# Optimization experiments

Measured on AMD Instinct MI355X. Metric: run time of the kernel, lower is better.

## Reference

```python
import jax, jax.numpy as jnp
import numpy as np

HEADS = 16
SEGS = 8


def _rotate_half(x):
    x1, x2 = jnp.split(x, 2, axis=-1)
    return jnp.concatenate([-x2, x1], axis=-1)


def _split_heads(t, h):
    b, n, dim = t.shape
    d = dim // h
    return t.reshape(b, n, h, d).transpose(0, 2, 1, 3).reshape(b * h, n, d)


def _merge_heads(t, b, h):
    c, n, d = t.shape
    return t.reshape(b, h, n, d).transpose(0, 2, 1, 3).reshape(b, n, h * d)


def setup_inputs() -> dict:
    key = jax.random.key(0)
    ks = jax.random.split(key, 5)
    b, n, dim = 2, 4096, 1024
    x = jax.random.normal(ks[0], (b, n, dim), dtype=jnp.float32)
    w = lambda k: jax.random.normal(k, (dim, dim), dtype=jnp.float32) * 0.02
    return {
        'x': x,
        'Wq': w(ks[1]),
        'Wkv': w(ks[2]),
        'Wo': w(ks[3]),
        'bo': jnp.zeros((dim,), jnp.float32),
        'Wo0': w(ks[4]),
        'bo0': jnp.zeros((dim,), jnp.float32),
    }


def reference(x, Wq, Wkv, Wo, bo, Wo0, bo0):
    b, n, dim = x.shape
    h = HEADS
    d = dim // h
    s = SEGS
    m = n // s  # segment_len
    mask_value = -jnp.finfo(x.dtype).max

    q = _split_heads(x @ Wq, h)    # (b*h, n, d)
    kv = _split_heads(x @ Wkv, h)  # (b*h, n, d)  (serves as both keys and values)

    # rotary embedding (layer_num == 0 branch)
    inv_freq = 1.0 / (10000.0 ** (jnp.arange(0, d, 2, dtype=jnp.float32) / d))
    freqs = jnp.arange(n, dtype=jnp.float32)[:, None] * inv_freq[None, :]  # (n, d/2)
    rot = jnp.concatenate([freqs, freqs], axis=-1)[None]  # (1, n, d)
    cos, sin = jnp.cos(rot), jnp.sin(rot)
    q = q * cos + _rotate_half(q) * sin
    kv = kv * cos + _rotate_half(kv) * sin

    q = q * (d ** -0.5)

    qs = q.reshape(-1, s, m, d)   # (c, s, m, d)
    kvs = kv.reshape(-1, s, m, d)

    # overlapping windows: segment t paired with segment t+1 as kv context
    kvs_ccs = jnp.concatenate([kvs[:, :-1], kvs[:, 1:]], axis=2)  # (c, s-1, 2m, d)
    qs_ccs = qs[:, 1:]                                            # (c, s-1, m, d)

    # NOTE: original computes lkv = LayerNorm(kvs_ccs) but never uses it (dead code) -> omitted.

    lsim = jnp.einsum('csmd,csnd->csmn', qs_ccs, kvs_ccs)  # (c, s-1, m, 2m)
    causal = jnp.triu(jnp.ones((m, m), dtype=bool), 1)
    # causal mask only applied to second half of keys (the own segment t+1)
    lsim = jnp.concatenate(
        [lsim[..., :m], jnp.where(causal, mask_value, lsim[..., m:])], axis=-1)

    attn0 = jnp.einsum('csmd,csnd->csmn', qs[:, :1], kvs[:, :1])  # (c, 1, m, m)
    attn0 = jnp.where(causal, mask_value, attn0)

    attn0 = jax.nn.softmax(attn0, axis=-1)
    attn1 = jax.nn.softmax(lsim, axis=-1)

    out0 = jnp.einsum('csij,csjd->csid', attn0, kvs[:, :1]).reshape(-1, m, d)
    out1 = jnp.einsum('csij,csjd->csid', attn1, kvs_ccs).reshape(-1, (s - 1) * m, d)

    out0 = _merge_heads(out0, b, h) @ Wo0 + bo0  # (b, m, dim)
    out1 = _merge_heads(out1, b, h) @ Wo + bo    # (b, (s-1)*m, dim)
    return jnp.concatenate([out0, out1], axis=1)  # (b, n, dim)
```

## Files before the change

### kernel.cpp

```cpp
#include <hip/hip_runtime.h>
#include <hip/hip_bf16.h>
#include <float.h>

using bf16 = __hip_bfloat16;
typedef __attribute__((ext_vector_type(8))) short bf16x8;
typedef __attribute__((ext_vector_type(4))) float f32x4;
typedef __attribute__((ext_vector_type(16))) float f32x16;

#define DIM   1024
#define NSEQ  4096
#define BATCH 2
#define NH    16
#define HD    64
#define NSEG  8
#define MSEG  512
#define ROWS  (BATCH*NSEQ)
#define NC    (BATCH*NH)
#define QSCALE (0.125f * 1.44269504f)

__device__ __forceinline__ float fast_exp2(float x) {
    float r;
    asm volatile("v_exp_f32 %0, %1" : "=v"(r) : "v"(x));
    return r;
}

__device__ __forceinline__ void gload16(const bf16* g, bf16* l) {
    __builtin_amdgcn_global_load_lds((const __attribute__((address_space(1))) unsigned int*)g,
                                     (__attribute__((address_space(3))) unsigned int*)l, 16, 0, 0);
}

__global__ void k_prep(const float* __restrict__ x, bf16* __restrict__ Xb,
                       const float* __restrict__ Wq, const float* __restrict__ Wkv,
                       const float* __restrict__ Wo, const float* __restrict__ Wo0,
                       bf16* __restrict__ WqT, bf16* __restrict__ WkvT,
                       bf16* __restrict__ WoT, bf16* __restrict__ Wo0T,
                       float* __restrict__ cosT, float* __restrict__ sinT) {
    __shared__ float tile[32][33];
    int b = blockIdx.x, tid = threadIdx.x;
    if (b < 8192) {
        int i = (b * 256 + tid) * 4;
        float4 v = *(const float4*)&x[i];
        union { bf16 h[4]; uint2 u; } p;
        p.h[0] = __float2bfloat16(v.x);
        p.h[1] = __float2bfloat16(v.y);
        p.h[2] = __float2bfloat16(v.z);
        p.h[3] = __float2bfloat16(v.w);
        *(uint2*)&Xb[i] = p.u;
    } else if (b < 12288) {
        int zz = (b - 8192) >> 10;
        int bb = (b - 8192) & 1023;
        int bxt = (bb & 31) * 32, byt = (bb >> 5) * 32;
        const float* W = (zz == 0) ? Wq : (zz == 1) ? Wkv : (zz == 2) ? Wo : Wo0;
        bf16* Wt = (zz == 0) ? WqT : (zz == 1) ? WkvT : (zz == 2) ? WoT : Wo0T;
        int tx = tid & 31, ty = tid >> 5;
        for (int ii = ty; ii < 32; ii += 8)
            tile[ii][tx] = W[(size_t)(byt + ii) * DIM + bxt + tx];
        __syncthreads();
        for (int ii = ty; ii < 32; ii += 8)
            Wt[(size_t)(bxt + ii) * DIM + byt + tx] = __float2bfloat16(tile[tx][ii]);
    } else {
        int idx = (b - 12288) * 256 + tid;
        int t = idx >> 5, ii = idx & 31;
        float freq = 1.0f / powf(10000.0f, (float)(2 * ii) * (1.0f / 64.0f));
        float a = (float)t * freq;
        cosT[idx] = cosf(a);
        sinT[idx] = sinf(a);
    }
}

__launch_bounds__(256, 3)
__global__ void k_gemm_qkv(const bf16* __restrict__ A, const bf16* __restrict__ Bq,
                           const bf16* __restrict__ Bkv, const float* __restrict__ cosT,
                           const float* __restrict__ sinT, bf16* __restrict__ Qb,
                           bf16* __restrict__ KVf) {
    __shared__ alignas(16) bf16 SH[24576];
    bf16* AsB = SH;
    bf16* BsB = SH + 12288;
    const int K = DIM;
    int tid = threadIdx.x;
    int lane = tid & 63, wave = tid >> 6;
    int hi = lane >> 5, lq = lane & 31;
    int wr = (wave >> 1) * 64, wc = (wave & 1) * 64;
    int id = blockIdx.x;
    int xcd = id & 7, rank = id >> 3;
    int by = xcd * 8 + (rank >> 4);
    int bxx = rank & 15;
    int m0 = by * 128;
    bool isQ = (bxx < 8);
    const bf16* Bt = isQ ? Bq : Bkv;
    int n0 = (bxx & 7) * 128;
    int row = lane & 15, kk = (lane >> 4) * 8;
    int kkA = kk ^ (((lane >> 1) & 3) << 3);
    int ch0 = wave * 128 + lane, ch1 = ch0 + 64;
    int r0 = ch0 >> 2, c0e = (ch0 & 3) * 8;
    int r1 = ch1 >> 2, c1e = (ch1 & 3) * 8;
    int c0s = c0e ^ (((r0 >> 1) & 3) << 3);
    int c1s = c1e ^ (((r1 >> 1) & 3) << 3);
    f32x4 acc[4][4] = {};

    auto stage = [&](int k0, int b) {
        gload16(&A[(size_t)(m0 + r0) * K + k0 + c0s], &AsB[b * 4096 + wave * 1024]);
        gload16(&A[(size_t)(m0 + r1) * K + k0 + c1s], &AsB[b * 4096 + wave * 1024 + 512]);
        gload16(&Bt[(size_t)(n0 + r0) * K + k0 + c0s], &BsB[b * 4096 + wave * 1024]);
        gload16(&Bt[(size_t)(n0 + r1) * K + k0 + c1s], &BsB[b * 4096 + wave * 1024 + 512]);
    };
    stage(0, 0);
    stage(32, 1);
    asm volatile("s_waitcnt vmcnt(4)" ::: "memory");
    __builtin_amdgcn_s_barrier();
    __builtin_amdgcn_sched_barrier(0);
    int cur = 0;
    for (int k = 0; k < 32; ++k) {
        if (k + 2 < 32) {
            int nb = cur + 2; if (nb >= 3) nb -= 3;
            stage(k * 32 + 64, nb);
        }
        bf16x8 af[4], bfr[4];
#pragma unroll
        for (int mt = 0; mt < 4; ++mt) af[mt] = *(const bf16x8*)&AsB[cur * 4096 + (wr + mt * 16 + row) * 32 + kkA];
#pragma unroll
        for (int nt = 0; nt < 4; ++nt) bfr[nt] = *(const bf16x8*)&BsB[cur * 4096 + (wc + nt * 16 + row) * 32 + kkA];
#pragma unroll
        for (int mt = 0; mt < 4; ++mt)
#pragma unroll
            for (int nt = 0; nt < 4; ++nt)
                acc[mt][nt] = __builtin_amdgcn_mfma_f32_16x16x32_bf16(af[mt], bfr[nt], acc[mt][nt], 0, 0, 0);
        if (k + 1 < 32) {
            if (k + 2 < 32) asm volatile("s_waitcnt vmcnt(4)" ::: "memory");
            else            asm volatile("s_waitcnt vmcnt(0)" ::: "memory");
            __builtin_amdgcn_s_barrier();
            __builtin_amdgcn_sched_barrier(0);
        }
        cur = cur + 1; if (cur == 3) cur = 0;
    }
    __syncthreads();
    bf16* Tw = SH + wave * (64 * 72);
    int orow = (lane >> 4) * 4, ocol = lane & 15;
    int head_g = (n0 + wc) >> 6;
    float sc = isQ ? QSCALE : 1.0f;
    int bidx = (m0 + wr) >> 12;
    int tbase = (m0 + wr) & (NSEQ - 1);
    int cch = bidx * NH + head_g;
#pragma unroll
    for (int mt = 0; mt < 4; ++mt) {
#pragma unroll
        for (int i = 0; i < 4; ++i) {
            int rl = mt * 16 + orow + i;
            int t = tbase + rl;
#pragma unroll
            for (int nt = 0; nt < 2; ++nt) {
                int e = nt * 16 + ocol;
                float x1 = acc[mt][nt][i], x2 = acc[mt][nt + 2][i];
                float cv = cosT[t * 32 + e], sv = sinT[t * 32 + e];
                Tw[rl * 72 + e]      = __float2bfloat16((x1 * cv - x2 * sv) * sc);
                Tw[rl * 72 + e + 32] = __float2bfloat16((x2 * cv + x1 * sv) * sc);
            }
        }
    }
    if (isQ) {
        int rsub = lane >> 3, dg = (lane & 7) * 8;
        size_t qbase = ((size_t)cch * NSEQ + tbase) * HD;
#pragma unroll
        for (int rr = 0; rr < 8; ++rr) {
            int rl = rr * 8 + rsub;
            *(uint4*)&Qb[qbase + (size_t)rl * HD + dg] = *(const uint4*)&Tw[rl * 72 + dg];
        }
    } else {
        size_t kvfbase = ((size_t)cch * 128 + (tbase >> 5)) * 4096;
#pragma unroll
        for (int st = 0; st < 2; ++st) {
            size_t tb = kvfbase + (size_t)st * 4096;
#pragma unroll
            for (int f = 0; f < 4; ++f)
                *(uint4*)&KVf[tb + f * 512 + lane * 8] =
                    *(const uint4*)&Tw[(st * 32 + lq) * 72 + f * 16 + hi * 8];
#pragma unroll
            for (int m = 0; m < 4; ++m) {
                int d0 = (m >> 1) * 32, sb = m & 1;
                union { bf16 h[8]; uint4 u; } pk;
#pragma unroll
                for (int j = 0; j < 8; ++j)
                    pk.h[j] = Tw[(st * 32 + sb * 16 + hi * 8 + j) * 72 + d0 + lq];
                *(uint4*)&KVf[tb + (size_t)(4 + m) * 512 + lane * 8] = pk.u;
            }
        }
    }
}

__launch_bounds__(256, 4)
__global__ void k_gemm_out(const bf16* __restrict__ A, const bf16* __restrict__ Bt0,
                           const bf16* __restrict__ Bt1, const float* __restrict__ bias0,
                           const float* __restrict__ bias1, float* __restrict__ C) {
    __shared__ alignas(16) bf16 As[3][128 * 32];
    __shared__ alignas(16) bf16 Bs[3][64 * 32];
    const int K = DIM;
    int tid = threadIdx.x;
    int lane = tid & 63, wave = tid >> 6;
    int wr = (wave >> 1) * 64, wc = (wave & 1) * 32;
    int id = blockIdx.x;
    int xcd = id & 7, rank = id >> 3;
    int by = xcd * 8 + (rank >> 4);
    int bx = rank & 15;
    int m0 = by * 128, n0 = bx * 64;
    bool first = (m0 & (NSEQ - 1)) < MSEG;
    const bf16* Bt = first ? Bt0 : Bt1;
    const float* bias = first ? bias0 : bias1;
    int row = lane & 15, kk = (lane >> 4) * 8;
    int kkA = kk ^ (((lane >> 1) & 3) << 3);
    int ch0 = wave * 128 + lane, ch1 = ch0 + 64;
    int r0 = ch0 >> 2, c0e = (ch0 & 3) * 8;
    int r1 = ch1 >> 2, c1e = (ch1 & 3) * 8;
    int c0s = c0e ^ (((r0 >> 1) & 3) << 3);
    int c1s = c1e ^ (((r1 >> 1) & 3) << 3);
    int cb = wave * 64 + lane;
    int rb = cb >> 2, cbe = (cb & 3) * 8;
    int cbs = cbe ^ (((rb >> 1) & 3) << 3);
    f32x4 acc[4][2] = {};

    auto stage = [&](int k0, int b) {
        gload16(&A[(size_t)(m0 + r0) * K + k0 + c0s], &As[b][wave * 1024]);
        gload16(&A[(size_t)(m0 + r1) * K + k0 + c1s], &As[b][wave * 1024 + 512]);
        gload16(&Bt[(size_t)(n0 + rb) * K + k0 + cbs], &Bs[b][wave * 512]);
    };
    stage(0, 0);
    stage(32, 1);
    asm volatile("s_waitcnt vmcnt(3)" ::: "memory");
    __builtin_amdgcn_s_barrier();
    __builtin_amdgcn_sched_barrier(0);
    int cur = 0;
    for (int k = 0; k < 32; ++k) {
        if (k + 2 < 32) {
            int nb = cur + 2; if (nb >= 3) nb -= 3;
            stage(k * 32 + 64, nb);
        }
        bf16x8 af[4], bfr[2];
#pragma unroll
        for (int mt = 0; mt < 4; ++mt) af[mt] = *(const bf16x8*)&As[cur][(wr + mt * 16 + row) * 32 + kkA];
#pragma unroll
        for (int nt = 0; nt < 2; ++nt) bfr[nt] = *(const bf16x8*)&Bs[cur][(wc + nt * 16 + row) * 32 + kkA];
#pragma unroll
        for (int mt = 0; mt < 4; ++mt)
#pragma unroll
            for (int nt = 0; nt < 2; ++nt)
                acc[mt][nt] = __builtin_amdgcn_mfma_f32_16x16x32_bf16(af[mt], bfr[nt], acc[mt][nt], 0, 0, 0);
        if (k + 1 < 32) {
            if (k + 2 < 32) asm volatile("s_waitcnt vmcnt(3)" ::: "memory");
            else            asm volatile("s_waitcnt vmcnt(0)" ::: "memory");
            __builtin_amdgcn_s_barrier();
            __builtin_amdgcn_sched_barrier(0);
        }
        cur = cur + 1; if (cur == 3) cur = 0;
    }
    int orow = (lane >> 4) * 4, ocol = lane & 15;
#pragma unroll
    for (int mt = 0; mt < 4; ++mt)
#pragma unroll
        for (int nt = 0; nt < 2; ++nt) {
            float bv = bias[n0 + wc + nt * 16 + ocol];
#pragma unroll
            for (int i = 0; i < 4; ++i)
                C[(size_t)(m0 + wr + mt * 16 + orow + i) * DIM + n0 + wc + nt * 16 + ocol] = acc[mt][nt][i] + bv;
        }
}

__launch_bounds__(256, 4)
__global__ void k_attn(const bf16* __restrict__ Qb, const bf16* __restrict__ KVf,
                       bf16* __restrict__ Ob) {
    int lane = threadIdx.x & 63, wave = threadIdx.x >> 6;
    int hi = lane >> 5, lq = lane & 31;
    int id = blockIdx.x;
    int xcd = id & 7, rank = id >> 3;
    int c = xcd * 4 + (rank & 3);
    int hr = rank >> 2;
    int bx, seg;
    if (hr < 28) { bx = 3 - hr / 7; seg = 1 + hr % 7; }
    else         { seg = 0; bx = 31 - hr; }
    int i0 = bx * 128 + wave * 32;
    int bidx = c >> 4, head = c & 15;
    int tq = seg * MSEG + i0 + lq;
    const bf16* qptr = &Qb[((size_t)c * NSEQ + tq) * HD + hi * 8];
    bf16x8 qf[4];
#pragma unroll
    for (int dc = 0; dc < 4; ++dc) qf[dc] = *(const bf16x8*)&qptr[dc * 16];
    f32x16 o0 = {}, o1 = {};
    float mrun = -FLT_MAX, lrun = 0.f;
    int kvbase = (seg == 0) ? 0 : (seg - 1) * MSEG;
    int cstart = (seg == 0) ? 0 : MSEG;
    int cend = cstart + i0 + 32;
    int nT = cend >> 5;

    const bf16* fb = &KVf[((size_t)c * 128 + (kvbase >> 5)) * 4096 + lane * 8];

    bf16x8 ka0, ka1, ka2, ka3;
    f32x16 s;
    {
        bf16x8 k0 = *(const bf16x8*)&fb[0];
        bf16x8 k1 = *(const bf16x8*)&fb[512];
        bf16x8 k2 = *(const bf16x8*)&fb[1024];
        bf16x8 k3 = *(const bf16x8*)&fb[1536];
        if (nT > 1) {
            const bf16* p1 = fb + 4096;
            ka0 = *(const bf16x8*)&p1[0];
            ka1 = *(const bf16x8*)&p1[512];
            ka2 = *(const bf16x8*)&p1[1024];
            ka3 = *(const bf16x8*)&p1[1536];
        }
        f32x16 z = {};
        __builtin_amdgcn_s_setprio(1);
        z = __builtin_amdgcn_mfma_f32_32x32x16_bf16(k0, qf[0], z, 0, 0, 0);
        z = __builtin_amdgcn_mfma_f32_32x32x16_bf16(k1, qf[1], z, 0, 0, 0);
        z = __builtin_amdgcn_mfma_f32_32x32x16_bf16(k2, qf[2], z, 0, 0, 0);
        z = __builtin_amdgcn_mfma_f32_32x32x16_bf16(k3, qf[3], z, 0, 0, 0);
        __builtin_amdgcn_s_setprio(0);
        s = z;
    }

    for (int it = 0; it < nT; ++it) {
        int c0 = it * 32;
        const bf16* pv = fb + (size_t)it * 4096 + 2048;
        bf16x8 vf0 = *(const bf16x8*)&pv[0];
        bf16x8 vf1 = *(const bf16x8*)&pv[512];
        bf16x8 vf2 = *(const bf16x8*)&pv[1024];
        bf16x8 vf3 = *(const bf16x8*)&pv[1536];
        if (c0 + 31 >= cstart && c0 + 31 - cstart > i0) {
#pragma unroll
            for (int r = 0; r < 16; ++r) {
                int kvg = c0 + ((r & 3) + 8 * (r >> 2) + 4 * hi);
                if (kvg >= cstart && kvg - cstart > i0 + lq) s[r] = -FLT_MAX;
            }
        }
        float m8[8], m4[4];
#pragma unroll
        for (int r = 0; r < 8; ++r) m8[r] = fmaxf(s[2 * r], s[2 * r + 1]);
#pragma unroll
        for (int r = 0; r < 4; ++r) m4[r] = fmaxf(m8[2 * r], m8[2 * r + 1]);
        float vmax = fmaxf(fmaxf(m4[0], m4[1]), fmaxf(m4[2], m4[3]));
        vmax = fmaxf(vmax, __shfl_xor(vmax, 32));
        if (__any(vmax > mrun + 11.5f)) {
            float nm = fmaxf(mrun, vmax);
            float al = fast_exp2(mrun - nm);
#pragma unroll
            for (int r = 0; r < 16; ++r) { o0[r] *= al; o1[r] *= al; }
            lrun *= al;
            mrun = nm;
        }
        float p[16];
#pragma unroll
        for (int r = 0; r < 16; ++r) p[r] = fast_exp2(s[r] - mrun);
        if (it + 1 < nT) {
            f32x16 z = {};
            __builtin_amdgcn_s_setprio(1);
            z = __builtin_amdgcn_mfma_f32_32x32x16_bf16(ka0, qf[0], z, 0, 0, 0);
            z = __builtin_amdgcn_mfma_f32_32x32x16_bf16(ka1, qf[1], z, 0, 0, 0);
            z = __builtin_amdgcn_mfma_f32_32x32x16_bf16(ka2, qf[2], z, 0, 0, 0);
            z = __builtin_amdgcn_mfma_f32_32x32x16_bf16(ka3, qf[3], z, 0, 0, 0);
            __builtin_amdgcn_s_setprio(0);
            s = z;
            if (it + 2 < nT) {
                const bf16* pn = fb + (size_t)(it + 2) * 4096;
                ka0 = *(const bf16x8*)&pn[0];
                ka1 = *(const bf16x8*)&pn[512];
                ka2 = *(const bf16x8*)&pn[1024];
                ka3 = *(const bf16x8*)&pn[1536];
            }
        }
        float a8[8], a4[4];
#pragma unroll
        for (int r = 0; r < 8; ++r) a8[r] = p[2 * r] + p[2 * r + 1];
#pragma unroll
        for (int r = 0; r < 4; ++r) a4[r] = a8[2 * r] + a8[2 * r + 1];
        lrun += (a4[0] + a4[1]) + (a4[2] + a4[3]);
        unsigned pk[8];
#pragma unroll
        for (int k = 0; k < 8; ++k) {
            union { bf16 h[2]; unsigned u; } cv;
            cv.h[0] = __float2bfloat16(p[2 * k]);
            cv.h[1] = __float2bfloat16(p[2 * k + 1]);
            pk[k] = cv.u;
        }
        unsigned u0 = hi ? pk[0] : pk[2];
        unsigned u1 = hi ? pk[1] : pk[3];
        unsigned u2 = hi ? pk[4] : pk[6];
        unsigned u3 = hi ? pk[5] : pk[7];
        unsigned w0 = (unsigned)__shfl_xor((int)u0, 32);
        unsigned w1 = (unsigned)__shfl_xor((int)u1, 32);
        unsigned w2 = (unsigned)__shfl_xor((int)u2, 32);
        unsigned w3 = (unsigned)__shfl_xor((int)u3, 32);
        union { unsigned u[4]; bf16x8 v; } b0, b1;
        b0.u[0] = hi ? w0 : pk[0];
        b0.u[1] = hi ? w1 : pk[1];
        b0.u[2] = hi ? pk[2] : w0;
        b0.u[3] = hi ? pk[3] : w1;
        b1.u[0] = hi ? w2 : pk[4];
        b1.u[1] = hi ? w3 : pk[5];
        b1.u[2] = hi ? pk[6] : w2;
        b1.u[3] = hi ? pk[7] : w3;
        __builtin_amdgcn_s_setprio(1);
        o0 = __builtin_amdgcn_mfma_f32_32x32x16_bf16(vf0, b0.v, o0, 0, 0, 0);
        o1 = __builtin_amdgcn_mfma_f32_32x32x16_bf16(vf2, b0.v, o1, 0, 0, 0);
        o0 = __builtin_amdgcn_mfma_f32_32x32x16_bf16(vf1, b1.v, o0, 0, 0, 0);
        o1 = __builtin_amdgcn_mfma_f32_32x32x16_bf16(vf3, b1.v, o1, 0, 0, 0);
        __builtin_amdgcn_s_setprio(0);
    }
    lrun += __shfl_xor(lrun, 32);
    float inv = 1.0f / lrun;
    size_t obase = ((size_t)bidx * NSEQ + tq) * DIM + head * HD;
#pragma unroll
    for (int dt = 0; dt < 2; ++dt)
#pragma unroll
        for (int a = 0; a < 4; ++a) {
            union { bf16 h[4]; uint2 u; } pkd;
            const f32x16& ov = dt ? o1 : o0;
#pragma unroll
            for (int i = 0; i < 4; ++i) pkd.h[i] = __float2bfloat16(ov[4 * a + i] * inv);
            *(uint2*)&Ob[obase + dt * 32 + 8 * a + 4 * hi] = pkd.u;
        }
}

extern "C" void kernel_launch(void* const* d_in, const int* in_sizes, int n_in,
                              void* d_out, int out_size, void* d_ws, size_t ws_size,
                              hipStream_t stream) {
    const float* x   = (const float*)d_in[0];
    const float* Wq  = (const float*)d_in[1];
    const float* Wkv = (const float*)d_in[2];
    const float* Wo  = (const float*)d_in[3];
    const float* bo  = (const float*)d_in[4];
    const float* Wo0 = (const float*)d_in[5];
    const float* bo0 = (const float*)d_in[6];
    float* out = (float*)d_out;

    char* ws = (char*)d_ws;
    size_t off = 0;
    auto alloc = [&](size_t bytes) { void* p = ws + off; off += (bytes + 255) & ~(size_t)255; return p; };
    float* cosT = (float*)alloc((size_t)NSEQ * 32 * 4);
    float* sinT = (float*)alloc((size_t)NSEQ * 32 * 4);
    bf16* Xb    = (bf16*)alloc((size_t)ROWS * DIM * 2);
    bf16* WqT   = (bf16*)alloc((size_t)DIM * DIM * 2);
    bf16* WkvT  = (bf16*)alloc((size_t)DIM * DIM * 2);
    bf16* WoT   = (bf16*)alloc((size_t)DIM * DIM * 2);
    bf16* Wo0T  = (bf16*)alloc((size_t)DIM * DIM * 2);
    bf16* Qb    = (bf16*)alloc((size_t)NC * NSEQ * HD * 2);
    bf16* KVf   = (bf16*)alloc((size_t)NC * 128 * 4096 * 2);
    bf16* Ob    = (bf16*)alloc((size_t)ROWS * DIM * 2);

    hipLaunchKernelGGL(k_prep, dim3(12800), dim3(256), 0, stream,
                       x, Xb, Wq, Wkv, Wo, Wo0, WqT, WkvT, WoT, Wo0T, cosT, sinT);

    hipLaunchKernelGGL(k_gemm_qkv, dim3(1024), dim3(256), 0, stream, Xb, WqT, WkvT, cosT, sinT, Qb, KVf);

    hipLaunchKernelGGL(k_attn, dim3(1024), dim3(256), 0, stream, Qb, KVf, Ob);

    hipLaunchKernelGGL(k_gemm_out, dim3(1024), dim3(256), 0, stream, Ob, Wo0T, WoT, bo0, bo, out);
}
```

Baseline: 142.6 us.

## Split attention KV range across wave pairs and merge partial softmax in LDS

Each block now covers two 32-row query tiles, and each tile's KV loop is split between two waves (split-K flash attention). The partial outputs, maxima and sums are combined through shared memory before the write. The grid doubles to 2048 blocks. The split shortens the longest serial chain per wave and evens out causal work imbalance. It also removes the software prefetch of the next K tile, so load latency is exposed inside the loop, and it adds LDS traffic and two barriers.

```diff
diff --git a/kernel.cpp b/kernel.cpp
--- a/kernel.cpp
+++ b/kernel.cpp
@@ -266,16 +266,21 @@
 __launch_bounds__(256, 4)
 __global__ void k_attn(const bf16* __restrict__ Qb, const bf16* __restrict__ KVf,
                        bf16* __restrict__ Ob) {
+    __shared__ float Osh[2][32][68];
+    __shared__ float Msh[4][32];
+    __shared__ float Lsh[4][32];
     int lane = threadIdx.x & 63, wave = threadIdx.x >> 6;
     int hi = lane >> 5, lq = lane & 31;
+    int half = wave >> 1, qsel = wave & 1;
     int id = blockIdx.x;
     int xcd = id & 7, rank = id >> 3;
     int c = xcd * 4 + (rank & 3);
     int hr = rank >> 2;
-    int bx, seg;
-    if (hr < 28) { bx = 3 - hr / 7; seg = 1 + hr % 7; }
-    else         { seg = 0; bx = 31 - hr; }
-    int i0 = bx * 128 + wave * 32;
+    int j, seg;
+    if (hr < 56) { j = 7 - hr / 7; seg = 1 + hr % 7; }
+    else         { seg = 0; j = 63 - hr; }
+    int qb = 2 * j + qsel;
+    int i0 = qb * 32;
     int bidx = c >> 4, head = c & 15;
     int tq = seg * MSEG + i0 + lq;
     const bf16* qptr = &Qb[((size_t)c * NSEQ + tq) * HD + hi * 8];
@@ -286,42 +291,31 @@
     float mrun = -FLT_MAX, lrun = 0.f;
     int kvbase = (seg == 0) ? 0 : (seg - 1) * MSEG;
     int cstart = (seg == 0) ? 0 : MSEG;
-    int cend = cstart + i0 + 32;
-    int nT = cend >> 5;
+    int nT = (cstart + i0 + 32) >> 5;
+    int hmid = (nT + 1) >> 1;
+    int h0 = half ? hmid : 0;
+    int h1 = half ? nT : hmid;
 
     const bf16* fb = &KVf[((size_t)c * 128 + (kvbase >> 5)) * 4096 + lane * 8];
 
-    bf16x8 ka0, ka1, ka2, ka3;
-    f32x16 s;
-    {
-        bf16x8 k0 = *(const bf16x8*)&fb[0];
-        bf16x8 k1 = *(const bf16x8*)&fb[512];
-        bf16x8 k2 = *(const bf16x8*)&fb[1024];
-        bf16x8 k3 = *(const bf16x8*)&fb[1536];
-        if (nT > 1) {
-            const bf16* p1 = fb + 4096;
-            ka0 = *(const bf16x8*)&p1[0];
-            ka1 = *(const bf16x8*)&p1[512];
-            ka2 = *(const bf16x8*)&p1[1024];
-            ka3 = *(const bf16x8*)&p1[1536];
-        }
-        f32x16 z = {};
+    for (int it = h0; it < h1; ++it) {
+        int c0 = it * 32;
+        const bf16* pt = fb + (size_t)it * 4096;
+        bf16x8 kf0 = *(const bf16x8*)&pt[0];
+        bf16x8 kf1 = *(const bf16x8*)&pt[512];
+        bf16x8 kf2 = *(const bf16x8*)&pt[1024];
+        bf16x8 kf3 = *(const bf16x8*)&pt[1536];
+        f32x16 s = {};
         __builtin_amdgcn_s_setprio(1);
-        z = __builtin_amdgcn_mfma_f32_32x32x16_bf16(k0, qf[0], z, 0, 0, 0);
-        z = __builtin_amdgcn_mfma_f32_32x32x16_bf16(k1, qf[1], z, 0, 0, 0);
-        z = __builtin_amdgcn_mfma_f32_32x32x16_bf16(k2, qf[2], z, 0, 0, 0);
-        z = __builtin_amdgcn_mfma_f32_32x32x16_bf16(k3, qf[3], z, 0, 0, 0);
+        s = __builtin_amdgcn_mfma_f32_32x32x16_bf16(kf0, qf[0], s, 0, 0, 0);
+        s = __builtin_amdgcn_mfma_f32_32x32x16_bf16(kf1, qf[1], s, 0, 0, 0);
+        s = __builtin_amdgcn_mfma_f32_32x32x16_bf16(kf2, qf[2], s, 0, 0, 0);
+        s = __builtin_amdgcn_mfma_f32_32x32x16_bf16(kf3, qf[3], s, 0, 0, 0);
         __builtin_amdgcn_s_setprio(0);
-        s = z;
-    }
-
-    for (int it = 0; it < nT; ++it) {
-        int c0 = it * 32;
-        const bf16* pv = fb + (size_t)it * 4096 + 2048;
-        bf16x8 vf0 = *(const bf16x8*)&pv[0];
-        bf16x8 vf1 = *(const bf16x8*)&pv[512];
-        bf16x8 vf2 = *(const bf16x8*)&pv[1024];
-        bf16x8 vf3 = *(const bf16x8*)&pv[1536];
+        bf16x8 vf0 = *(const bf16x8*)&pt[2048];
+        bf16x8 vf1 = *(const bf16x8*)&pt[2560];
+        bf16x8 vf2 = *(const bf16x8*)&pt[3072];
+        bf16x8 vf3 = *(const bf16x8*)&pt[3584];
         if (c0 + 31 >= cstart && c0 + 31 - cstart > i0) {
 #pragma unroll
             for (int r = 0; r < 16; ++r) {
@@ -347,23 +341,6 @@
         float p[16];
 #pragma unroll
         for (int r = 0; r < 16; ++r) p[r] = fast_exp2(s[r] - mrun);
-        if (it + 1 < nT) {
-            f32x16 z = {};
-            __builtin_amdgcn_s_setprio(1);
-            z = __builtin_amdgcn_mfma_f32_32x32x16_bf16(ka0, qf[0], z, 0, 0, 0);
-            z = __builtin_amdgcn_mfma_f32_32x32x16_bf16(ka1, qf[1], z, 0, 0, 0);
-            z = __builtin_amdgcn_mfma_f32_32x32x16_bf16(ka2, qf[2], z, 0, 0, 0);
-            z = __builtin_amdgcn_mfma_f32_32x32x16_bf16(ka3, qf[3], z, 0, 0, 0);
-            __builtin_amdgcn_s_setprio(0);
-            s = z;
-            if (it + 2 < nT) {
-                const bf16* pn = fb + (size_t)(it + 2) * 4096;
-                ka0 = *(const bf16x8*)&pn[0];
-                ka1 = *(const bf16x8*)&pn[512];
-                ka2 = *(const bf16x8*)&pn[1024];
-                ka3 = *(const bf16x8*)&pn[1536];
-            }
-        }
         float a8[8], a4[4];
 #pragma unroll
         for (int r = 0; r < 8; ++r) a8[r] = p[2 * r] + p[2 * r + 1];
@@ -403,18 +380,41 @@
         __builtin_amdgcn_s_setprio(0);
     }
     lrun += __shfl_xor(lrun, 32);
-    float inv = 1.0f / lrun;
-    size_t obase = ((size_t)bidx * NSEQ + tq) * DIM + head * HD;
-#pragma unroll
-    for (int dt = 0; dt < 2; ++dt)
-#pragma unroll
-        for (int a = 0; a < 4; ++a) {
-            union { bf16 h[4]; uint2 u; } pkd;
-            const f32x16& ov = dt ? o1 : o0;
-#pragma unroll
-            for (int i = 0; i < 4; ++i) pkd.h[i] = __float2bfloat16(ov[4 * a + i] * inv);
-            *(uint2*)&Ob[obase + dt * 32 + 8 * a + 4 * hi] = pkd.u;
-        }
+    if (lane < 32) { Msh[wave][lq] = mrun; Lsh[wave][lq] = lrun; }
+    __syncthreads();
+    float mp = Msh[wave ^ 2][lq];
+    float M = fmaxf(mrun, mp);
+    float scl = fast_exp2(mrun - M);
+    if (half == 0) {
+#pragma unroll
+        for (int r = 0; r < 16; ++r) {
+            int d = (r & 3) + 8 * (r >> 2) + 4 * hi;
+            Osh[qsel][lq][d]      = o0[r] * scl;
+            Osh[qsel][lq][d + 32] = o1[r] * scl;
+        }
+    }
+    __syncthreads();
+    if (half == 1) {
+        float lt = lrun * scl + Lsh[wave ^ 2][lq] * fast_exp2(mp - M);
+        float inv = 1.0f / lt;
+#pragma unroll
+        for (int r = 0; r < 16; ++r) {
+            int d = (r & 3) + 8 * (r >> 2) + 4 * hi;
+            o0[r] = o0[r] * scl + Osh[qsel][lq][d];
+            o1[r] = o1[r] * scl + Osh[qsel][lq][d + 32];
+        }
+        size_t obase = ((size_t)bidx * NSEQ + tq) * DIM + head * HD;
+#pragma unroll
+        for (int dt = 0; dt < 2; ++dt)
+#pragma unroll
+            for (int a = 0; a < 4; ++a) {
+                union { bf16 h[4]; uint2 u; } pkd;
+                const f32x16& ov = dt ? o1 : o0;
+#pragma unroll
+                for (int i = 0; i < 4; ++i) pkd.h[i] = __float2bfloat16(ov[4 * a + i] * inv);
+                *(uint2*)&Ob[obase + dt * 32 + 8 * a + 4 * hi] = pkd.u;
+            }
+    }
 }
 
 extern "C" void kernel_launch(void* const* d_in, const int* in_sizes, int n_in,
@@ -448,7 +448,7 @@
 
     hipLaunchKernelGGL(k_gemm_qkv, dim3(1024), dim3(256), 0, stream, Xb, WqT, WkvT, cosT, sinT, Qb, KVf);
 
-    hipLaunchKernelGGL(k_attn, dim3(1024), dim3(256), 0, stream, Qb, KVf, Ob);
+    hipLaunchKernelGGL(k_attn, dim3(2048), dim3(256), 0, stream, Qb, KVf, Ob);
 
     hipLaunchKernelGGL(k_gemm_out, dim3(1024), dim3(256), 0, stream, Ob, Wo0T, WoT, bo0, bo, out);
 }
```

Result: faster. 138.3 us (-2.9%).
